# Performance work log

Measured on AMD Instinct MI355X. Metric: run time of the kernel, lower is better.

Reference implementation:

```python
import jax, jax.numpy as jnp
import numpy as np


def _conv1d(x, w, b):
    # x: (B, Cin, T_padded), w: (Cout, Cin, K), b: (Cout,) -> (B, Cout, T_out)
    y = jax.lax.conv_general_dilated(
        x, w, window_strides=(1,), padding='VALID',
        dimension_numbers=('NCH', 'OIH', 'NCH'))
    return y + b[None, :, None]


def setup_inputs() -> dict:
    key = jax.random.key(0)
    ks = jax.random.split(key, 7)
    B, C, T, H = 32, 64, 8192, 256
    W = 0.05  # small init scale (xavier-ish, keeps exp(log_s) stable)
    return {
        'x': jax.random.normal(ks[0], (B, C, T), dtype=jnp.float32),
        'w_in': jax.random.normal(ks[1], (H, C, 3), dtype=jnp.float32) * W,
        'b_in': jax.random.normal(ks[2], (H,), dtype=jnp.float32) * W,
        'w_mid': jax.random.normal(ks[3], (H, H, 3), dtype=jnp.float32) * W,
        'b_mid': jax.random.normal(ks[4], (H,), dtype=jnp.float32) * W,
        'w_out': jax.random.normal(ks[5], (2 * C, H, 3), dtype=jnp.float32) * W,
        'b_out': jax.random.normal(ks[6], (2 * C,), dtype=jnp.float32) * W,
        'alpha': jnp.ones((1, C, 1), dtype=jnp.float32),
        'beta': jnp.zeros((1, C, 1), dtype=jnp.float32),
    }


def reference(x, w_in, b_in, w_mid, b_mid, w_out, b_out, alpha, beta):
    C = x.shape[1]
    # causal shift: drop last timestep, left-pad 3 -> conv(k=3) yields T outputs
    x_in = jnp.pad(x[:, :, :-1], ((0, 0), (0, 0), (3, 0)))
    rs = _conv1d(x_in, w_in, b_in)                                  # (B, H, T)
    rs = _conv1d(jnp.pad(rs, ((0, 0), (0, 0), (2, 0))), w_mid, b_mid)
    rs = _conv1d(jnp.pad(rs, ((0, 0), (0, 0), (2, 0))), w_out, b_out)  # (B, 2C, T)
    log_s, t = rs[:, :C, :], rs[:, C:, :]
    log_s = alpha * jnp.tanh(log_s) + beta
    z = jnp.exp(log_s) * x + t
    return z
```

## Files before the change

### kernel.cpp

```cpp
#include <hip/hip_runtime.h>
#include <cmath>

typedef __attribute__((ext_vector_type(8)))  short short8;
typedef __attribute__((ext_vector_type(4)))  float f32x4;
typedef __attribute__((ext_vector_type(16))) float f32x16;

#define B_   32
#define C_   64
#define T_   8192
#define H_   256
#define TT   128

#define RS_ROWB 528
#define XS_ROWB 144
#define BUF_OFF 0
#define XS_OFF  77088
#define LDS_BYTES (77088 + 162*144)

#define A1_SZ  98304
#define A2_SZ  393216
#define A3_SZ  196608
#define AW_TOTAL (A1_SZ + A2_SZ + A3_SZ)

__device__ __forceinline__ unsigned short f2bf(float f) {
    unsigned u = __builtin_bit_cast(unsigned, f);
    u += 0x7fffu + ((u >> 16) & 1u);
    return (unsigned short)(u >> 16);
}
__device__ __forceinline__ unsigned cvtpk(float lo, float hi) {
    unsigned r;
    asm("v_cvt_pk_bf16_f32 %0, %1, %2" : "=v"(r) : "v"(lo), "v"(hi));
    return r;
}

__global__ void pack_w(const float* __restrict__ w1, const float* __restrict__ w2,
                       const float* __restrict__ w3, unsigned short* __restrict__ ws)
{
    int id = blockIdx.x * 256 + threadIdx.x;
    const float* w; int MT, KT, Cin; unsigned short* dst;
    if (id < 6144)       {             w = w1; MT = 8; KT = 4;  Cin = 64;  dst = ws; }
    else if (id < 30720) { id -= 6144; w = w2; MT = 8; KT = 16; Cin = 256; dst = ws + A1_SZ/2; }
    else if (id < 43008) { id -= 30720; w = w3; MT = 4; KT = 16; Cin = 256; dst = ws + (A1_SZ+A2_SZ)/2; }
    else return;
    const int lane = id & 63;
    int f = id >> 6;
    const int kt = f % KT; f /= KT;
    const int mt = f % MT;
    const int tap = f / MT;
    const int h  = mt*32 + (lane & 31);
    const int c0 = kt*16 + (lane >> 5)*8;
    unsigned short* o = dst + (size_t)id * 8;
    #pragma unroll
    for (int j = 0; j < 8; ++j)
        o[j] = f2bf(w[((size_t)(h*Cin + c0 + j))*3 + tap]);
}

__device__ __forceinline__ short8 ldA(const char* base, int frag, int lane) {
    return *(const short8*)(base + ((size_t)frag*64 + lane)*16);
}

__global__ __launch_bounds__(512, 2)
void arflow_mfma(const float* __restrict__ x,
                 const float* __restrict__ b_in, const float* __restrict__ b_mid,
                 const float* __restrict__ b_out,
                 const float* __restrict__ alpha, const float* __restrict__ beta,
                 const char* __restrict__ wpk,
                 float* __restrict__ out)
{
    __shared__ __align__(16) char lds[LDS_BYTES];
    unsigned short* xs = (unsigned short*)(lds + XS_OFF);
    char* buf = lds + BUF_OFF;

    const char* wA1 = wpk;
    const char* wA2 = wpk + A1_SZ;
    const char* wA3 = wpk + A1_SZ + A2_SZ;

    const int b   = blockIdx.y;
    const int t0  = blockIdx.x * TT;
    const int tid = threadIdx.x;
    const int lane = tid & 63;
    const int wid  = tid >> 6;
    const int l31 = lane & 31, l5 = lane >> 5;

    {
        const int rr = tid & 127, cg = tid >> 7;
        const int t = t0 - 19 + rr;
        #pragma unroll
        for (int p = 0; p < 8; ++p) {
            const int c = cg*16 + p*2;
            const float* xc0 = x + ((size_t)b*C_ + c)*T_;
            const float* xc1 = xc0 + T_;
            float v0 = 0.f, v1 = 0.f;
            if (t >= 0) { v0 = xc0[t]; v1 = xc1[t]; }
            *(unsigned*)(&xs[rr*72 + c]) = cvtpk(v0, v1);
            if (rr < 19) {
                const int t2 = t + 128;
                *(unsigned*)(&xs[(rr+128)*72 + c]) = cvtpk(xc0[t2], xc1[t2]);
            }
        }
    }
    __syncthreads();

    {
        const int mt = wid;
        f32x4 bq[4];
        #pragma unroll
        for (int q = 0; q < 4; ++q)
            bq[q] = *(const f32x4*)(b_in + mt*32 + q*8 + l5*4);
        f32x16 acc[5];
        #pragma unroll
        for (int nt = 0; nt < 5; ++nt)
            #pragma unroll
            for (int q = 0; q < 4; ++q) {
                acc[nt][4*q+0] = bq[q][0]; acc[nt][4*q+1] = bq[q][1];
                acc[nt][4*q+2] = bq[q][2]; acc[nt][4*q+3] = bq[q][3];
            }
        int nb[5];
        #pragma unroll
        for (int nt = 0; nt < 5; ++nt)
            nb[nt] = XS_OFF + (32*nt + l31)*XS_ROWB + l5*16;

        short8 Ar[4];
        short8 Br[2][5];
        #pragma unroll
        for (int k = 0; k < 3; ++k)
            Ar[k] = ldA(wA1, ((k>>2)*8 + mt)*4 + (k&3), lane);
        #pragma unroll
        for (int nt = 0; nt < 5; ++nt)
            Br[0][nt] = *(const short8*)(lds + nb[nt]);
        #pragma unroll
        for (int kt = 0; kt < 12; ++kt) {
            if (kt + 3 < 12) {
                const int kn = kt + 3;
                Ar[(kt+3)&3] = ldA(wA1, ((kn>>2)*8 + mt)*4 + (kn&3), lane);
            }
            if (kt + 1 < 12) {
                const int kn = kt + 1, tapn = kn >> 2, ckn = kn & 3;
                #pragma unroll
                for (int nt = 0; nt < 5; ++nt)
                    Br[(kt+1)&1][nt] = *(const short8*)(lds + nb[nt] + tapn*XS_ROWB + ckn*32);
            }
            __builtin_amdgcn_s_setprio(1);
            #pragma unroll
            for (int nt = 0; nt < 5; ++nt)
                acc[nt] = __builtin_amdgcn_mfma_f32_32x32x16_bf16(Ar[kt&3], Br[kt&1][nt], acc[nt], 0, 0, 0);
            __builtin_amdgcn_s_setprio(0);
        }
        #pragma unroll
        for (int nt = 0; nt < 5; ++nt) {
            const int rb = 2 + 32*nt + l31;
            const int t  = t0 - 16 + 32*nt + l31;
            if (rb <= 145) {
                char* dst0 = buf + rb*RS_ROWB + mt*64;
                #pragma unroll
                for (int q = 0; q < 4; ++q) {
                    unsigned long long pk = 0ull;
                    if (t >= 0)
                        pk = (unsigned long long)cvtpk(acc[nt][4*q+0], acc[nt][4*q+1])
                           | ((unsigned long long)cvtpk(acc[nt][4*q+2], acc[nt][4*q+3]) << 32);
                    *(unsigned long long*)(dst0 + q*16 + l5*8) = pk;
                }
            }
        }
    }
    __syncthreads();

    {
        const int mg = wid >> 1, ng = wid & 1;
        const int mt0 = mg*2;
        const int ntb = ng ? 3 : 0, ncnt = ng ? 2 : 3;
        f32x16 acc[2][3];
        #pragma unroll
        for (int m = 0; m < 2; ++m) {
            f32x4 bq[4];
            #pragma unroll
            for (int q = 0; q < 4; ++q)
                bq[q] = *(const f32x4*)(b_mid + (mt0+m)*32 + q*8 + l5*4);
            #pragma unroll
            for (int nt = 0; nt < 3; ++nt)
                #pragma unroll
                for (int q = 0; q < 4; ++q) {
                    acc[m][nt][4*q+0] = bq[q][0]; acc[m][nt][4*q+1] = bq[q][1];
                    acc[m][nt][4*q+2] = bq[q][2]; acc[m][nt][4*q+3] = bq[q][3];
                }
        }
        int nb[3];
        #pragma unroll
        for (int nt = 0; nt < 3; ++nt)
            nb[nt] = BUF_OFF + (14 + 32*(ntb+nt) + l31)*RS_ROWB + l5*16;

        short8 Ar[4][2];
        short8 Br[2][3];
        #pragma unroll
        for (int k = 0; k < 3; ++k) {
            const int tap = k >> 4, ck = k & 15;
            #pragma unroll
            for (int m = 0; m < 2; ++m)
                Ar[k][m] = ldA(wA2, (tap*8 + mt0+m)*16 + ck, lane);
        }
        #pragma unroll
        for (int nt = 0; nt < 3; ++nt) if (nt < ncnt)
            Br[0][nt] = *(const short8*)(lds + nb[nt]);
        #pragma unroll
        for (int kt = 0; kt < 48; ++kt) {
            if (kt + 3 < 48) {
                const int kn = kt + 3, tapn = kn >> 4, ckn = kn & 15;
                #pragma unroll
                for (int m = 0; m < 2; ++m)
                    Ar[(kt+3)&3][m] = ldA(wA2, (tapn*8 + mt0+m)*16 + ckn, lane);
            }
            if (kt + 1 < 48) {
                const int kn = kt + 1, tapn = kn >> 4, ckn = kn & 15;
                #pragma unroll
                for (int nt = 0; nt < 3; ++nt) if (nt < ncnt)
                    Br[(kt+1)&1][nt] = *(const short8*)(lds + nb[nt] + tapn*RS_ROWB + ckn*32);
            }
            __builtin_amdgcn_s_setprio(1);
            #pragma unroll
            for (int nt = 0; nt < 3; ++nt) if (nt < ncnt) {
                #pragma unroll
                for (int m = 0; m < 2; ++m)
                    acc[m][nt] = __builtin_amdgcn_mfma_f32_32x32x16_bf16(Ar[kt&3][m], Br[kt&1][nt], acc[m][nt], 0, 0, 0);
            }
            __builtin_amdgcn_s_setprio(0);
        }
        __syncthreads();
        #pragma unroll
        for (int nt = 0; nt < 3; ++nt) if (nt < ncnt) {
            const int r2 = 32*(ntb+nt) + l31;
            const int t  = t0 - 2 + r2;
            if (r2 <= 129) {
                #pragma unroll
                for (int m = 0; m < 2; ++m) {
                    char* dst0 = buf + r2*RS_ROWB + (mt0+m)*64;
                    #pragma unroll
                    for (int q = 0; q < 4; ++q) {
                        unsigned long long pk = 0ull;
                        if (t >= 0)
                            pk = (unsigned long long)cvtpk(acc[m][nt][4*q+0], acc[m][nt][4*q+1])
                               | ((unsigned long long)cvtpk(acc[m][nt][4*q+2], acc[m][nt][4*q+3]) << 32);
                        *(unsigned long long*)(dst0 + q*16 + l5*8) = pk;
                    }
                }
            }
        }
    }

    float xv[16];
    #pragma unroll
    for (int m = 0; m < 16; ++m) {
        const int e = tid + m*512;
        const int c = e >> 7, tl = e & 127;
        xv[m] = x[((size_t)b*C_ + c)*T_ + t0 + tl];
    }
    __syncthreads();

    {
        const int mt = wid & 3, ng = wid >> 2;
        const int ntb = ng*2;
        f32x4 bq[4];
        #pragma unroll
        for (int q = 0; q < 4; ++q)
            bq[q] = *(const f32x4*)(b_out + mt*32 + q*8 + l5*4);
        f32x16 acc[2];
        #pragma unroll
        for (int nt = 0; nt < 2; ++nt)
            #pragma unroll
            for (int q = 0; q < 4; ++q) {
                acc[nt][4*q+0] = bq[q][0]; acc[nt][4*q+1] = bq[q][1];
                acc[nt][4*q+2] = bq[q][2]; acc[nt][4*q+3] = bq[q][3];
            }
        int nb[2];
        #pragma unroll
        for (int nt = 0; nt < 2; ++nt)
            nb[nt] = BUF_OFF + (32*(ntb+nt) + l31)*RS_ROWB + l5*16;

        short8 Ar[6];
        short8 Br[2][2];
        #pragma unroll
        for (int k = 0; k < 5; ++k) {
            const int tap = k >> 4, ck = k & 15;
            Ar[k] = ldA(wA3, (tap*4 + mt)*16 + ck, lane);
        }
        #pragma unroll
        for (int nt = 0; nt < 2; ++nt)
            Br[0][nt] = *(const short8*)(lds + nb[nt]);
        #pragma unroll
        for (int kt = 0; kt < 48; ++kt) {
            if (kt + 5 < 48) {
                const int kn = kt + 5, tapn = kn >> 4, ckn = kn & 15;
                Ar[(kt+5)%6] = ldA(wA3, (tapn*4 + mt)*16 + ckn, lane);
            }
            if (kt + 1 < 48) {
                const int kn = kt + 1, tapn = kn >> 4, ckn = kn & 15;
                #pragma unroll
                for (int nt = 0; nt < 2; ++nt)
                    Br[(kt+1)&1][nt] = *(const short8*)(lds + nb[nt] + tapn*RS_ROWB + ckn*32);
            }
            __builtin_amdgcn_s_setprio(1);
            #pragma unroll
            for (int nt = 0; nt < 2; ++nt)
                acc[nt] = __builtin_amdgcn_mfma_f32_32x32x16_bf16(Ar[kt%6], Br[kt&1][nt], acc[nt], 0, 0, 0);
            __builtin_amdgcn_s_setprio(0);
        }
        __syncthreads();
        #pragma unroll
        for (int nt = 0; nt < 2; ++nt) {
            const int row = 32*(ntb+nt) + l31;
            char* dst0 = buf + row*RS_ROWB + mt*128;
            #pragma unroll
            for (int q = 0; q < 4; ++q) {
                f32x4 v;
                v[0] = acc[nt][4*q+0]; v[1] = acc[nt][4*q+1];
                v[2] = acc[nt][4*q+2]; v[3] = acc[nt][4*q+3];
                *(f32x4*)(dst0 + q*32 + l5*16) = v;
            }
        }
    }
    __syncthreads();

    {
        const float* rs3f = (const float*)buf;
        #pragma unroll
        for (int m = 0; m < 16; ++m) {
            const int e = tid + m*512;
            const int c = e >> 7, tl = e & 127;
            const float ls = rs3f[tl*132 + c];
            const float tv = rs3f[tl*132 + c + 64];
            const float e2 = __expf(2.f * ls);
            const float th = fmaf(-2.f, __builtin_amdgcn_rcpf(e2 + 1.f), 1.f);
            const float lsv = fmaf(alpha[c], th, beta[c]);
            out[((size_t)b*C_ + c)*T_ + t0 + tl] = fmaf(__expf(lsv), xv[m], tv);
        }
    }
}

extern "C" void kernel_launch(void* const* d_in, const int* in_sizes, int n_in,
                              void* d_out, int out_size, void* d_ws, size_t ws_size,
                              hipStream_t stream) {
    const float* x     = (const float*)d_in[0];
    const float* w_in  = (const float*)d_in[1];
    const float* b_in  = (const float*)d_in[2];
    const float* w_mid = (const float*)d_in[3];
    const float* b_mid = (const float*)d_in[4];
    const float* w_out = (const float*)d_in[5];
    const float* b_out = (const float*)d_in[6];
    const float* alpha = (const float*)d_in[7];
    const float* beta  = (const float*)d_in[8];
    float* out = (float*)d_out;

    if (ws_size < (size_t)AW_TOTAL) return;

    hipLaunchKernelGGL(pack_w, dim3(168), dim3(256), 0, stream,
                       w_in, w_mid, w_out, (unsigned short*)d_ws);
    hipLaunchKernelGGL(arflow_mfma, dim3(T_/TT, B_), dim3(512), 0, stream,
                       x, b_in, b_mid, b_out, alpha, beta, (const char*)d_ws, out);
}
```

Before: 216.0 us.

## Use 768-thread blocks with 12 waves and rebalanced per-stage MFMA tiling

Raises the block from 8 to 12 waves and changes launch bounds to 3 blocks per CU. The three conv stages are re-partitioned over a 4x3 wave grid: stage 1 uses 2 M-tiles by up to 2 N-tiles per wave, stage 2 drops from 3 to 2 N-tiles per wave, and stage 3 gives the first N-group two tiles and the others one. The input staging and the epilogue loops are remapped to the new thread count, and zeroing of the first buffer row is added. The intent is more waves in flight to hide latency, at the cost of register pressure from the tighter launch bound and uneven work across the N-groups.

```diff
diff --git a/kernel.cpp b/kernel.cpp
--- a/kernel.cpp
+++ b/kernel.cpp
@@ -10,6 +10,7 @@
 #define T_   8192
 #define H_   256
 #define TT   128
+#define NTH  768
 
 #define RS_ROWB 528
 #define XS_ROWB 144
@@ -59,7 +60,7 @@
     return *(const short8*)(base + ((size_t)frag*64 + lane)*16);
 }
 
-__global__ __launch_bounds__(512, 2)
+__global__ __launch_bounds__(NTH, 3)
 void arflow_mfma(const float* __restrict__ x,
                  const float* __restrict__ b_in, const float* __restrict__ b_mid,
                  const float* __restrict__ b_out,
@@ -81,116 +82,130 @@
     const int lane = tid & 63;
     const int wid  = tid >> 6;
     const int l31 = lane & 31, l5 = lane >> 5;
-
-    {
-        const int rr = tid & 127, cg = tid >> 7;
-        const int t = t0 - 19 + rr;
-        #pragma unroll
-        for (int p = 0; p < 8; ++p) {
-            const int c = cg*16 + p*2;
-            const float* xc0 = x + ((size_t)b*C_ + c)*T_;
-            const float* xc1 = xc0 + T_;
-            float v0 = 0.f, v1 = 0.f;
-            if (t >= 0) { v0 = xc0[t]; v1 = xc1[t]; }
-            *(unsigned*)(&xs[rr*72 + c]) = cvtpk(v0, v1);
-            if (rr < 19) {
-                const int t2 = t + 128;
-                *(unsigned*)(&xs[(rr+128)*72 + c]) = cvtpk(xc0[t2], xc1[t2]);
-            }
-        }
+    const int mg = wid & 3;
+    const int ng = wid >> 2;
+
+    {
+        const int cg = tid / 192;
+        const int tt = tid - cg*192;
+        if (tt < 147) {
+            const int t = t0 - 19 + tt;
+            #pragma unroll
+            for (int p = 0; p < 8; ++p) {
+                const int c = cg*16 + p*2;
+                const float* xc0 = x + ((size_t)b*C_ + c)*T_;
+                const float* xc1 = xc0 + T_;
+                float v0 = 0.f, v1 = 0.f;
+                if (t >= 0) { v0 = xc0[t]; v1 = xc1[t]; }
+                *(unsigned*)(&xs[tt*72 + c]) = cvtpk(v0, v1);
+            }
+        }
+        if (tid < 264) ((unsigned*)buf)[tid] = 0u;
     }
     __syncthreads();
 
     {
-        const int mt = wid;
-        f32x4 bq[4];
-        #pragma unroll
-        for (int q = 0; q < 4; ++q)
-            bq[q] = *(const f32x4*)(b_in + mt*32 + q*8 + l5*4);
-        f32x16 acc[5];
-        #pragma unroll
-        for (int nt = 0; nt < 5; ++nt)
-            #pragma unroll
-            for (int q = 0; q < 4; ++q) {
-                acc[nt][4*q+0] = bq[q][0]; acc[nt][4*q+1] = bq[q][1];
-                acc[nt][4*q+2] = bq[q][2]; acc[nt][4*q+3] = bq[q][3];
-            }
-        int nb[5];
-        #pragma unroll
-        for (int nt = 0; nt < 5; ++nt)
-            nb[nt] = XS_OFF + (32*nt + l31)*XS_ROWB + l5*16;
-
-        short8 Ar[4];
-        short8 Br[2][5];
-        #pragma unroll
-        for (int k = 0; k < 3; ++k)
-            Ar[k] = ldA(wA1, ((k>>2)*8 + mt)*4 + (k&3), lane);
-        #pragma unroll
-        for (int nt = 0; nt < 5; ++nt)
-            Br[0][nt] = *(const short8*)(lds + nb[nt]);
-        #pragma unroll
-        for (int kt = 0; kt < 12; ++kt) {
-            if (kt + 3 < 12) {
-                const int kn = kt + 3;
-                Ar[(kt+3)&3] = ldA(wA1, ((kn>>2)*8 + mt)*4 + (kn&3), lane);
-            }
-            if (kt + 1 < 12) {
-                const int kn = kt + 1, tapn = kn >> 2, ckn = kn & 3;
-                #pragma unroll
-                for (int nt = 0; nt < 5; ++nt)
-                    Br[(kt+1)&1][nt] = *(const short8*)(lds + nb[nt] + tapn*XS_ROWB + ckn*32);
-            }
-            __builtin_amdgcn_s_setprio(1);
-            #pragma unroll
-            for (int nt = 0; nt < 5; ++nt)
-                acc[nt] = __builtin_amdgcn_mfma_f32_32x32x16_bf16(Ar[kt&3], Br[kt&1][nt], acc[nt], 0, 0, 0);
-            __builtin_amdgcn_s_setprio(0);
-        }
-        #pragma unroll
-        for (int nt = 0; nt < 5; ++nt) {
-            const int rb = 2 + 32*nt + l31;
-            const int t  = t0 - 16 + 32*nt + l31;
-            if (rb <= 145) {
-                char* dst0 = buf + rb*RS_ROWB + mt*64;
-                #pragma unroll
-                for (int q = 0; q < 4; ++q) {
-                    unsigned long long pk = 0ull;
-                    if (t >= 0)
-                        pk = (unsigned long long)cvtpk(acc[nt][4*q+0], acc[nt][4*q+1])
-                           | ((unsigned long long)cvtpk(acc[nt][4*q+2], acc[nt][4*q+3]) << 32);
-                    *(unsigned long long*)(dst0 + q*16 + l5*8) = pk;
-                }
-            }
-        }
-    }
-    __syncthreads();
-
-    {
-        const int mg = wid >> 1, ng = wid & 1;
         const int mt0 = mg*2;
-        const int ntb = ng ? 3 : 0, ncnt = ng ? 2 : 3;
-        f32x16 acc[2][3];
+        const int ntb = ng*2, ncnt = (ng == 2) ? 1 : 2;
+        f32x16 acc[2][2];
         #pragma unroll
         for (int m = 0; m < 2; ++m) {
             f32x4 bq[4];
             #pragma unroll
             for (int q = 0; q < 4; ++q)
-                bq[q] = *(const f32x4*)(b_mid + (mt0+m)*32 + q*8 + l5*4);
-            #pragma unroll
-            for (int nt = 0; nt < 3; ++nt)
+                bq[q] = *(const f32x4*)(b_in + (mt0+m)*32 + q*8 + l5*4);
+            #pragma unroll
+            for (int nt = 0; nt < 2; ++nt)
                 #pragma unroll
                 for (int q = 0; q < 4; ++q) {
                     acc[m][nt][4*q+0] = bq[q][0]; acc[m][nt][4*q+1] = bq[q][1];
                     acc[m][nt][4*q+2] = bq[q][2]; acc[m][nt][4*q+3] = bq[q][3];
                 }
         }
-        int nb[3];
-        #pragma unroll
-        for (int nt = 0; nt < 3; ++nt)
+        int nb[2];
+        #pragma unroll
+        for (int nt = 0; nt < 2; ++nt)
+            nb[nt] = XS_OFF + (32*(ntb+nt) + l31)*XS_ROWB + l5*16;
+
+        short8 Ar[4][2];
+        short8 Br[2][2];
+        #pragma unroll
+        for (int k = 0; k < 3; ++k)
+            #pragma unroll
+            for (int m = 0; m < 2; ++m)
+                Ar[k][m] = ldA(wA1, ((k>>2)*8 + mt0+m)*4 + (k&3), lane);
+        #pragma unroll
+        for (int nt = 0; nt < 2; ++nt) if (nt < ncnt)
+            Br[0][nt] = *(const short8*)(lds + nb[nt]);
+        #pragma unroll
+        for (int kt = 0; kt < 12; ++kt) {
+            if (kt + 3 < 12) {
+                const int kn = kt + 3;
+                #pragma unroll
+                for (int m = 0; m < 2; ++m)
+                    Ar[(kt+3)&3][m] = ldA(wA1, ((kn>>2)*8 + mt0+m)*4 + (kn&3), lane);
+            }
+            if (kt + 1 < 12) {
+                const int kn = kt + 1, tapn = kn >> 2, ckn = kn & 3;
+                #pragma unroll
+                for (int nt = 0; nt < 2; ++nt) if (nt < ncnt)
+                    Br[(kt+1)&1][nt] = *(const short8*)(lds + nb[nt] + tapn*XS_ROWB + ckn*32);
+            }
+            __builtin_amdgcn_s_setprio(1);
+            #pragma unroll
+            for (int nt = 0; nt < 2; ++nt) if (nt < ncnt)
+                #pragma unroll
+                for (int m = 0; m < 2; ++m)
+                    acc[m][nt] = __builtin_amdgcn_mfma_f32_32x32x16_bf16(Ar[kt&3][m], Br[kt&1][nt], acc[m][nt], 0, 0, 0);
+            __builtin_amdgcn_s_setprio(0);
+        }
+        #pragma unroll
+        for (int nt = 0; nt < 2; ++nt) if (nt < ncnt) {
+            const int rb = 2 + 32*(ntb+nt) + l31;
+            const int t  = t0 - 16 + 32*(ntb+nt) + l31;
+            if (rb <= 145) {
+                #pragma unroll
+                for (int m = 0; m < 2; ++m) {
+                    char* dst0 = buf + rb*RS_ROWB + (mt0+m)*64;
+                    #pragma unroll
+                    for (int q = 0; q < 4; ++q) {
+                        unsigned long long pk = 0ull;
+                        if (t >= 0)
+                            pk = (unsigned long long)cvtpk(acc[m][nt][4*q+0], acc[m][nt][4*q+1])
+                               | ((unsigned long long)cvtpk(acc[m][nt][4*q+2], acc[m][nt][4*q+3]) << 32);
+                        *(unsigned long long*)(dst0 + q*16 + l5*8) = pk;
+                    }
+                }
+            }
+        }
+    }
+    __syncthreads();
+
+    {
+        const int mt0 = mg*2;
+        const int ntb = ng*2, ncnt = (ng == 2) ? 1 : 2;
+        f32x16 acc[2][2];
+        #pragma unroll
+        for (int m = 0; m < 2; ++m) {
+            f32x4 bq[4];
+            #pragma unroll
+            for (int q = 0; q < 4; ++q)
+                bq[q] = *(const f32x4*)(b_mid + (mt0+m)*32 + q*8 + l5*4);
+            #pragma unroll
+            for (int nt = 0; nt < 2; ++nt)
+                #pragma unroll
+                for (int q = 0; q < 4; ++q) {
+                    acc[m][nt][4*q+0] = bq[q][0]; acc[m][nt][4*q+1] = bq[q][1];
+                    acc[m][nt][4*q+2] = bq[q][2]; acc[m][nt][4*q+3] = bq[q][3];
+                }
+        }
+        int nb[2];
+        #pragma unroll
+        for (int nt = 0; nt < 2; ++nt)
             nb[nt] = BUF_OFF + (14 + 32*(ntb+nt) + l31)*RS_ROWB + l5*16;
 
         short8 Ar[4][2];
-        short8 Br[2][3];
+        short8 Br[2][2];
         #pragma unroll
         for (int k = 0; k < 3; ++k) {
             const int tap = k >> 4, ck = k & 15;
@@ -199,7 +214,7 @@
                 Ar[k][m] = ldA(wA2, (tap*8 + mt0+m)*16 + ck, lane);
         }
         #pragma unroll
-        for (int nt = 0; nt < 3; ++nt) if (nt < ncnt)
+        for (int nt = 0; nt < 2; ++nt) if (nt < ncnt)
             Br[0][nt] = *(const short8*)(lds + nb[nt]);
         #pragma unroll
         for (int kt = 0; kt < 48; ++kt) {
@@ -212,21 +227,20 @@
             if (kt + 1 < 48) {
                 const int kn = kt + 1, tapn = kn >> 4, ckn = kn & 15;
                 #pragma unroll
-                for (int nt = 0; nt < 3; ++nt) if (nt < ncnt)
+                for (int nt = 0; nt < 2; ++nt) if (nt < ncnt)
                     Br[(kt+1)&1][nt] = *(const short8*)(lds + nb[nt] + tapn*RS_ROWB + ckn*32);
             }
             __builtin_amdgcn_s_setprio(1);
             #pragma unroll
-            for (int nt = 0; nt < 3; ++nt) if (nt < ncnt) {
+            for (int nt = 0; nt < 2; ++nt) if (nt < ncnt)
                 #pragma unroll
                 for (int m = 0; m < 2; ++m)
                     acc[m][nt] = __builtin_amdgcn_mfma_f32_32x32x16_bf16(Ar[kt&3][m], Br[kt&1][nt], acc[m][nt], 0, 0, 0);
-            }
             __builtin_amdgcn_s_setprio(0);
         }
         __syncthreads();
         #pragma unroll
-        for (int nt = 0; nt < 3; ++nt) if (nt < ncnt) {
+        for (int nt = 0; nt < 2; ++nt) if (nt < ncnt) {
             const int r2 = 32*(ntb+nt) + l31;
             const int t  = t0 - 2 + r2;
             if (r2 <= 129) {
@@ -246,18 +260,21 @@
         }
     }
 
-    float xv[16];
+    float xv[11];
     #pragma unroll
-    for (int m = 0; m < 16; ++m) {
-        const int e = tid + m*512;
-        const int c = e >> 7, tl = e & 127;
-        xv[m] = x[((size_t)b*C_ + c)*T_ + t0 + tl];
+    for (int m = 0; m < 11; ++m) {
+        const int e = tid + m*NTH;
+        if (e < 8192) {
+            const int c = e >> 7, tl = e & 127;
+            xv[m] = x[((size_t)b*C_ + c)*T_ + t0 + tl];
+        }
     }
     __syncthreads();
 
     {
-        const int mt = wid & 3, ng = wid >> 2;
-        const int ntb = ng*2;
+        const int mt = mg;
+        const int ntb = (ng == 0) ? 0 : (ng + 1);
+        const int ncnt = (ng == 0) ? 2 : 1;
         f32x4 bq[4];
         #pragma unroll
         for (int q = 0; q < 4; ++q)
@@ -283,7 +300,7 @@
             Ar[k] = ldA(wA3, (tap*4 + mt)*16 + ck, lane);
         }
         #pragma unroll
-        for (int nt = 0; nt < 2; ++nt)
+        for (int nt = 0; nt < 2; ++nt) if (nt < ncnt)
             Br[0][nt] = *(const short8*)(lds + nb[nt]);
         #pragma unroll
         for (int kt = 0; kt < 48; ++kt) {
@@ -294,18 +311,18 @@
             if (kt + 1 < 48) {
                 const int kn = kt + 1, tapn = kn >> 4, ckn = kn & 15;
                 #pragma unroll
-                for (int nt = 0; nt < 2; ++nt)
+                for (int nt = 0; nt < 2; ++nt) if (nt < ncnt)
                     Br[(kt+1)&1][nt] = *(const short8*)(lds + nb[nt] + tapn*RS_ROWB + ckn*32);
             }
             __builtin_amdgcn_s_setprio(1);
             #pragma unroll
-            for (int nt = 0; nt < 2; ++nt)
+            for (int nt = 0; nt < 2; ++nt) if (nt < ncnt)
                 acc[nt] = __builtin_amdgcn_mfma_f32_32x32x16_bf16(Ar[kt%6], Br[kt&1][nt], acc[nt], 0, 0, 0);
             __builtin_amdgcn_s_setprio(0);
         }
         __syncthreads();
         #pragma unroll
-        for (int nt = 0; nt < 2; ++nt) {
+        for (int nt = 0; nt < 2; ++nt) if (nt < ncnt) {
             const int row = 32*(ntb+nt) + l31;
             char* dst0 = buf + row*RS_ROWB + mt*128;
             #pragma unroll
@@ -322,15 +339,17 @@
     {
         const float* rs3f = (const float*)buf;
         #pragma unroll
-        for (int m = 0; m < 16; ++m) {
-            const int e = tid + m*512;
-            const int c = e >> 7, tl = e & 127;
-            const float ls = rs3f[tl*132 + c];
-            const float tv = rs3f[tl*132 + c + 64];
-            const float e2 = __expf(2.f * ls);
-            const float th = fmaf(-2.f, __builtin_amdgcn_rcpf(e2 + 1.f), 1.f);
-            const float lsv = fmaf(alpha[c], th, beta[c]);
-            out[((size_t)b*C_ + c)*T_ + t0 + tl] = fmaf(__expf(lsv), xv[m], tv);
+        for (int m = 0; m < 11; ++m) {
+            const int e = tid + m*NTH;
+            if (e < 8192) {
+                const int c = e >> 7, tl = e & 127;
+                const float ls = rs3f[tl*132 + c];
+                const float tv = rs3f[tl*132 + c + 64];
+                const float e2 = __expf(2.f * ls);
+                const float th = fmaf(-2.f, __builtin_amdgcn_rcpf(e2 + 1.f), 1.f);
+                const float lsv = fmaf(alpha[c], th, beta[c]);
+                out[((size_t)b*C_ + c)*T_ + t0 + tl] = fmaf(__expf(lsv), xv[m], tv);
+            }
         }
     }
 }
@@ -353,6 +372,6 @@
 
     hipLaunchKernelGGL(pack_w, dim3(168), dim3(256), 0, stream,
                        w_in, w_mid, w_out, (unsigned short*)d_ws);
-    hipLaunchKernelGGL(arflow_mfma, dim3(T_/TT, B_), dim3(512), 0, stream,
+    hipLaunchKernelGGL(arflow_mfma, dim3(T_/TT, B_), dim3(NTH), 0, stream,
                        x, b_in, b_mid, b_out, alpha, beta, (const char*)d_ws, out);
 }
```

New measurement: 252.5 us. 1.17x slower.
